# Kernel tuning notes

Hardware: AMD Instinct MI355X
Metric: run time of the kernel (lower is better)

## Reference

```python
import jax, jax.numpy as jnp
import numpy as np

NUM_QUBITS = 6
DIM = 2 ** NUM_QUBITS  # 64


def _u_gate(theta, phi, lam):
    # qiskit U(theta, phi, lam)
    c = jnp.cos(theta / 2).astype(jnp.complex64)
    s = jnp.sin(theta / 2).astype(jnp.complex64)
    ephi = jnp.exp(1j * phi.astype(jnp.complex64))
    elam = jnp.exp(1j * lam.astype(jnp.complex64))
    return jnp.stack([
        jnp.stack([c, -elam * s]),
        jnp.stack([ephi * s, ephi * elam * c]),
    ])


def _p_gate(lam):
    one = jnp.ones((), jnp.complex64)
    return jnp.stack([
        jnp.stack([one, jnp.zeros((), jnp.complex64)]),
        jnp.stack([jnp.zeros((), jnp.complex64), jnp.exp(1j * lam.astype(jnp.complex64))]),
    ])


def _controlled(U):
    # 4x4 matrix in |control, target> basis: block-diag(I2, U)
    return jnp.eye(4, dtype=jnp.complex64).at[2:, 2:].set(U)


_CX = jnp.array([[1, 0, 0, 0], [0, 1, 0, 0], [0, 0, 0, 1], [0, 0, 1, 0]], dtype=jnp.complex64)


def _apply_1q(psi, U, q):
    # psi: (B, 2,2,2,2,2,2); qubit q (qiskit little-endian) -> axis 6-q
    ax = NUM_QUBITS - q
    psi = jnp.moveaxis(psi, ax, -1)
    psi = psi @ U.T
    return jnp.moveaxis(psi, -1, ax)


def _apply_2q(psi, G, qa, qb):
    # G is 4x4 acting on (qa, qb) with index 2*bit(qa)+bit(qb)
    a, b = NUM_QUBITS - qa, NUM_QUBITS - qb
    psi = jnp.moveaxis(psi, (a, b), (-2, -1))
    shp = psi.shape
    psi = (psi.reshape(shp[:-2] + (4,)) @ G.T).reshape(shp)
    return jnp.moveaxis(psi, (-2, -1), (a, b))


def _circuit(features, params):
    # amplitude encoding (qc.initialize with L2 normalization; |0> fallback for zero vec)
    norm = jnp.linalg.norm(features, axis=1, keepdims=True)
    safe = jnp.where(jnp.isclose(norm, 0.0), 1.0, norm)
    e0 = jnp.zeros((1, DIM), features.dtype).at[0, 0].set(1.0)
    psi = jnp.where(jnp.isclose(norm, 0.0), e0, features / safe)
    psi = psi.astype(jnp.complex64).reshape((-1,) + (2,) * NUM_QUBITS)

    def U3(i):
        return _u_gate(params[i], params[i + 1], params[i + 2])

    # layer 1: U on all qubits (params 0..17)
    for q in range(NUM_QUBITS):
        psi = _apply_1q(psi, U3(3 * q), q)
    # cx(2,1); p(18,1); cx(4,3); p(19,3)
    psi = _apply_2q(psi, _CX, 2, 1)
    psi = _apply_1q(psi, _p_gate(params[18]), 1)
    psi = _apply_2q(psi, _CX, 4, 3)
    psi = _apply_1q(psi, _p_gate(params[19]), 3)
    # layer 2: U on [0,1,3,5] (params 20..31)
    idx = 20
    for q in [0, 1, 3, 5]:
        psi = _apply_1q(psi, U3(idx), q)
        idx += 3
    # controlled-U(32..34) ctrl 0 -> tgt 1; controlled-U(35..37) ctrl 3 -> tgt 5
    psi = _apply_2q(psi, _controlled(U3(32)), 0, 1)
    psi = _apply_2q(psi, _controlled(U3(35)), 3, 5)
    # cx(3,1); p(38,1)
    psi = _apply_2q(psi, _CX, 3, 1)
    psi = _apply_1q(psi, _p_gate(params[38]), 1)
    # final: U on [0,1] (39..44); CU(45..47) ctrl 0 -> tgt 1; U on [0,1] (48..53)
    psi = _apply_1q(psi, U3(39), 0)
    psi = _apply_1q(psi, U3(42), 1)
    psi = _apply_2q(psi, _controlled(U3(45)), 0, 1)
    psi = _apply_1q(psi, U3(48), 0)
    psi = _apply_1q(psi, U3(51), 1)

    # observable kron(diag(1,-1), I_32): +1 for index < 32, -1 otherwise (Z on qubit 5)
    probs = jnp.abs(psi.reshape(-1, DIM)) ** 2
    sign = jnp.where(jnp.arange(DIM) < DIM // 2, 1.0, -1.0).astype(jnp.float32)
    return (probs @ sign).astype(jnp.float32)


def setup_inputs() -> dict:
    key = jax.random.key(0)
    kf, kp = jax.random.split(key)
    features = jax.random.normal(kf, (262144, 64), dtype=jnp.float32)
    params = jax.random.uniform(kp, (54,), dtype=jnp.float32) * (0.1 * np.pi)
    return {"features": features, "params": params}


def reference(features, params):
    return _circuit(features, params)
```

## Files before the change

kernel.cpp:

```cpp
#include <hip/hip_runtime.h>

using f32x4  = __attribute__((ext_vector_type(4))) float;
using bf16x8 = __attribute__((ext_vector_type(8))) short;

__device__ inline unsigned short f2bf(float x) {
  unsigned u = __builtin_bit_cast(unsigned, x);
  return (unsigned short)((u + 0x7FFFu + ((u >> 16) & 1u)) >> 16);
}
__device__ inline float2 cmul(float2 a, float2 b) {
  return make_float2(a.x * b.x - a.y * b.y, a.x * b.y + a.y * b.x);
}
__device__ inline float2 cadd(float2 a, float2 b) { return make_float2(a.x + b.x, a.y + b.y); }

__device__ inline void gate1q(float2* psi, int t, int sub, int q,
                              float2 u00, float2 u01, float2 u10, float2 u11) {
  const int bit = 1 << q, mask = bit - 1;
#pragma unroll
  for (int pp = 0; pp < 8; ++pp) {
    int p  = sub * 8 + pp;
    int i0 = ((p & ~mask) << 1) | (p & mask);
    int i1 = i0 | bit;
    float2 a0 = psi[i0 * 64 + t], a1 = psi[i1 * 64 + t];
    psi[i0 * 64 + t] = cadd(cmul(u00, a0), cmul(u01, a1));
    psi[i1 * 64 + t] = cadd(cmul(u10, a0), cmul(u11, a1));
  }
}

__device__ inline void gatec(float2* psi, int t, int sub, int c, int g,
                             float2 v00, float2 v01, float2 v10, float2 v11) {
  const int cb = 1 << c, gb = 1 << g;
  const int lo = (c < g ? c : g), hi = (c < g ? g : c);
  const int mlo = (1 << lo) - 1, mhi = (1 << hi) - 1;
#pragma unroll
  for (int pp = 0; pp < 4; ++pp) {
    int p = sub * 4 + pp;
    int y = ((p & ~mlo) << 1) | (p & mlo);
    y     = ((y & ~mhi) << 1) | (y & mhi);
    int i0 = y | cb;
    int i1 = i0 | gb;
    float2 a0 = psi[i0 * 64 + t], a1 = psi[i1 * 64 + t];
    psi[i0 * 64 + t] = cadd(cmul(v00, a0), cmul(v01, a1));
    psi[i1 * 64 + t] = cadd(cmul(v10, a0), cmul(v11, a1));
  }
}

#define MFMA(A, B, C) __builtin_amdgcn_mfma_f32_16x16x32_bf16(A, B, C, 0, 0, 0)

__global__ __launch_bounds__(256, 3) void qfused(const float* __restrict__ F,
                                                 const float* __restrict__ Pp,
                                                 float* __restrict__ out) {
  __shared__ float2 psi[64 * 64];
  __shared__ __attribute__((aligned(16))) unsigned short Plds[128 * 64];
  __shared__ float tS[54], tC[54], tSh[54], tCh[54];
  __shared__ float sA00;

  const int tid = threadIdx.x;
  const int t = tid & 63, sub = tid >> 6;

  if (tid < 54) {
    float p = Pp[tid];
    tS[tid]  = __sinf(p);
    tC[tid]  = __cosf(p);
    tSh[tid] = __sinf(0.5f * p);
    tCh[tid] = __cosf(0.5f * p);
  }
  for (int idx = tid; idx < 4096; idx += 256)
    psi[idx] = make_float2(((idx >> 6) == (idx & 63)) ? 1.f : 0.f, 0.f);
  __syncthreads();

  float2 u00, u01, u10, u11;
  const float2 Z = make_float2(0.f, 0.f), ONE = make_float2(1.f, 0.f);
  auto U3L = [&](int i) {
    float ch = tCh[i], sh = tSh[i];
    float cp = tC[i + 1], sp = tS[i + 1];
    float cl = tC[i + 2], sl = tS[i + 2];
    u00 = make_float2(ch, 0.f);
    u01 = make_float2(-cl * sh, -sl * sh);
    u10 = make_float2(cp * sh, sp * sh);
    u11 = make_float2((cp * cl - sp * sl) * ch, (cp * sl + sp * cl) * ch);
  };
  auto PH = [&](int i) { return make_float2(tC[i], tS[i]); };

#pragma unroll
  for (int q = 0; q < 6; ++q) {
    U3L(3 * q); gate1q(psi, t, sub, q, u00, u01, u10, u11); __syncthreads();
  }
  gatec(psi, t, sub, 2, 1, Z, ONE, ONE, Z); __syncthreads();
  gate1q(psi, t, sub, 1, ONE, Z, Z, PH(18)); __syncthreads();
  gatec(psi, t, sub, 4, 3, Z, ONE, ONE, Z); __syncthreads();
  gate1q(psi, t, sub, 3, ONE, Z, Z, PH(19)); __syncthreads();
  const int qs[4] = {0, 1, 3, 5};
#pragma unroll
  for (int ii = 0; ii < 4; ++ii) {
    U3L(20 + 3 * ii); gate1q(psi, t, sub, qs[ii], u00, u01, u10, u11); __syncthreads();
  }
  U3L(32); gatec(psi, t, sub, 0, 1, u00, u01, u10, u11); __syncthreads();
  U3L(35); gatec(psi, t, sub, 3, 5, u00, u01, u10, u11); __syncthreads();
  gatec(psi, t, sub, 3, 1, Z, ONE, ONE, Z); __syncthreads();
  gate1q(psi, t, sub, 1, ONE, Z, Z, PH(38)); __syncthreads();
  U3L(39); gate1q(psi, t, sub, 0, u00, u01, u10, u11); __syncthreads();
  U3L(42); gate1q(psi, t, sub, 1, u00, u01, u10, u11); __syncthreads();
  U3L(45); gatec(psi, t, sub, 0, 1, u00, u01, u10, u11); __syncthreads();
  U3L(48); gate1q(psi, t, sub, 0, u00, u01, u10, u11); __syncthreads();
  U3L(51); gate1q(psi, t, sub, 1, u00, u01, u10, u11); __syncthreads();

  if (tid < 64) {
    float2 v = psi[tid * 64];
    float term = (v.x * v.x + v.y * v.y) * (tid < 32 ? 1.f : -1.f);
#pragma unroll
    for (int m = 1; m < 64; m <<= 1) term += __shfl_xor(term, m, 64);
    if (tid == 0) sA00 = term;
  }
  for (int idx = tid; idx < 8192; idx += 256) {
    int r = idx >> 6, j = idx & 63;
    int i = (r < 32) ? r : (r < 96) ? (r - 32) : (r - 64);
    bool im = (r >= 32 && r < 64) || (r >= 96);
    float2 v = psi[i * 64 + j];
    Plds[idx] = f2bf(im ? v.y : v.x);
  }
  __syncthreads();

  const int lane = tid & 63, wid = sub;
  const int g = lane >> 4, c0 = lane & 15;
  const unsigned short* pb = Plds + c0 * 64 + g * 8;
  bf16x8 Bf[8][2];
#pragma unroll
  for (int mt = 0; mt < 8; ++mt) {
    Bf[mt][0] = *(const bf16x8*)(pb + mt * 1024);
    Bf[mt][1] = *(const bf16x8*)(pb + mt * 1024 + 32);
  }
  const float A00 = sA00;

  const int gid   = (int)blockIdx.x * 4 + wid;
  const int start = gid * 5 + (gid < 1024 ? gid : 1024);
  const int count = 5 + (gid < 1024 ? 1 : 0);
  const float* fp = F + (size_t)start * 1024 + (size_t)c0 * 64 + g * 8;

#define LOADT(i, V0, V1, V2, V3) { const float* q_ = fp + (size_t)(i) * 1024; \
    V0 = *(const float4*)(q_); V1 = *(const float4*)(q_ + 4); \
    V2 = *(const float4*)(q_ + 32); V3 = *(const float4*)(q_ + 36); }

#define PROCESS(i, V0, V1, V2, V3) { \
    bf16x8 a0, a1; \
    a0[0] = f2bf(V0.x); a0[1] = f2bf(V0.y); a0[2] = f2bf(V0.z); a0[3] = f2bf(V0.w); \
    a0[4] = f2bf(V1.x); a0[5] = f2bf(V1.y); a0[6] = f2bf(V1.z); a0[7] = f2bf(V1.w); \
    a1[0] = f2bf(V2.x); a1[1] = f2bf(V2.y); a1[2] = f2bf(V2.z); a1[3] = f2bf(V2.w); \
    a1[4] = f2bf(V3.x); a1[5] = f2bf(V3.y); a1[6] = f2bf(V3.z); a1[7] = f2bf(V3.w); \
    f32x4 acc[8]; \
    _Pragma("unroll") \
    for (int mt = 0; mt < 8; ++mt) { \
      acc[mt] = (f32x4){0.f, 0.f, 0.f, 0.f}; \
      acc[mt] = MFMA(Bf[mt][0], a0, acc[mt]); \
      acc[mt] = MFMA(Bf[mt][1], a1, acc[mt]); \
    } \
    float sp_ = 0.f, sm_ = 0.f; \
    _Pragma("unroll") \
    for (int mt = 0; mt < 4; ++mt) { \
      _Pragma("unroll") \
      for (int r = 0; r < 4; ++r) { \
        sp_ = fmaf(acc[mt][r], acc[mt][r], sp_); \
        sm_ = fmaf(acc[mt + 4][r], acc[mt + 4][r], sm_); \
      } \
    } \
    sp_ += __shfl_xor(sp_, 16, 64); sm_ += __shfl_xor(sm_, 16, 64); \
    sp_ += __shfl_xor(sp_, 32, 64); sm_ += __shfl_xor(sm_, 32, 64); \
    if (lane < 16) { \
      float den = sp_ + sm_; \
      out[(size_t)(start + (i)) * 16 + c0] = (den < 1e-30f) ? A00 : (sp_ - sm_) / den; \
    } }

  float4 x0, x1, x2, x3, y0, y1, y2, y3;
  LOADT(0, x0, x1, x2, x3);
#pragma unroll
  for (int i = 0; i < 6; i += 2) {
    if (i >= count) break;
    const bool has2 = (i + 1 < count);
    if (has2) LOADT(i + 1, y0, y1, y2, y3);
    PROCESS(i, x0, x1, x2, x3);
    if (i + 2 < count) LOADT(i + 2, x0, x1, x2, x3);
    if (has2) PROCESS(i + 1, y0, y1, y2, y3);
  }
#undef LOADT
#undef PROCESS
}

extern "C" void kernel_launch(void* const* d_in, const int* in_sizes, int n_in,
                              void* d_out, int out_size, void* d_ws, size_t ws_size,
                              hipStream_t stream) {
  const float* F = (const float*)d_in[0];
  const float* P = (const float*)d_in[1];
  float* out = (float*)d_out;
  qfused<<<768, 256, 0, stream>>>(F, P, out);
}
```

Baseline: 114.3 us.

## Split circuit simulation into single-block kernel and fuse gates into 4x4 unitaries

Before this change, every one of the 768 blocks simulated the full 64x64 circuit unitary. Now one block does it once and writes the bf16 matrix and A00 to global memory, and a second kernel does the MFMA expectation pass. The first layer of 1-qubit gates becomes a closed-form Kronecker product, and neighbouring gate groups are merged into combined 4x4 two-qubit gates, which cuts the number of barriers and LDS passes. The cost is a second kernel launch and a serial single-block step before the main kernel, which now reads the matrix from global memory.

Result: no change. 112.9 us (-1.2%).

```diff
diff --git a/kernel.cpp b/kernel.cpp
--- a/kernel.cpp
+++ b/kernel.cpp
@@ -2,134 +2,177 @@
 
 using f32x4  = __attribute__((ext_vector_type(4))) float;
 using bf16x8 = __attribute__((ext_vector_type(8))) short;
+
+__device__ __attribute__((aligned(16))) unsigned short g_P[128 * 64];
+__device__ float g_A00;
 
 __device__ inline unsigned short f2bf(float x) {
   unsigned u = __builtin_bit_cast(unsigned, x);
   return (unsigned short)((u + 0x7FFFu + ((u >> 16) & 1u)) >> 16);
 }
-__device__ inline float2 cmul(float2 a, float2 b) {
-  return make_float2(a.x * b.x - a.y * b.y, a.x * b.y + a.y * b.x);
-}
-__device__ inline float2 cadd(float2 a, float2 b) { return make_float2(a.x + b.x, a.y + b.y); }
-
-__device__ inline void gate1q(float2* psi, int t, int sub, int q,
-                              float2 u00, float2 u01, float2 u10, float2 u11) {
-  const int bit = 1 << q, mask = bit - 1;
-#pragma unroll
-  for (int pp = 0; pp < 8; ++pp) {
-    int p  = sub * 8 + pp;
-    int i0 = ((p & ~mask) << 1) | (p & mask);
-    int i1 = i0 | bit;
-    float2 a0 = psi[i0 * 64 + t], a1 = psi[i1 * 64 + t];
-    psi[i0 * 64 + t] = cadd(cmul(u00, a0), cmul(u01, a1));
-    psi[i1 * 64 + t] = cadd(cmul(u10, a0), cmul(u11, a1));
-  }
-}
-
-__device__ inline void gatec(float2* psi, int t, int sub, int c, int g,
-                             float2 v00, float2 v01, float2 v10, float2 v11) {
-  const int cb = 1 << c, gb = 1 << g;
-  const int lo = (c < g ? c : g), hi = (c < g ? g : c);
+__device__ inline float2 cmul(float2 x, float2 y) {
+  return make_float2(x.x * y.x - x.y * y.y, x.x * y.y + x.y * y.x);
+}
+__device__ inline float2 cfma(float2 x, float2 y, float2 a) {
+  return make_float2(fmaf(x.x, y.x, fmaf(-x.y, y.y, a.x)),
+                     fmaf(x.x, y.y, fmaf(x.y, y.x, a.y)));
+}
+
+struct u2 { float2 a, b, c, d; };
+struct c4 { float2 m[4][4]; };
+
+__device__ inline u2 mk3(const float* tS, const float* tC,
+                         const float* tSh, const float* tCh, int i) {
+  float ch = tCh[i], sh = tSh[i];
+  float cp = tC[i + 1], sp = tS[i + 1];
+  float cl = tC[i + 2], sl = tS[i + 2];
+  u2 r;
+  r.a = make_float2(ch, 0.f);
+  r.b = make_float2(-cl * sh, -sl * sh);
+  r.c = make_float2(cp * sh, sp * sh);
+  r.d = make_float2((cp * cl - sp * sl) * ch, (cp * sl + sp * cl) * ch);
+  return r;
+}
+__device__ inline c4 kron2(const u2& A, const u2& B) {
+  c4 r;
+  r.m[0][0]=cmul(A.a,B.a); r.m[0][1]=cmul(A.a,B.b); r.m[0][2]=cmul(A.b,B.a); r.m[0][3]=cmul(A.b,B.b);
+  r.m[1][0]=cmul(A.a,B.c); r.m[1][1]=cmul(A.a,B.d); r.m[1][2]=cmul(A.b,B.c); r.m[1][3]=cmul(A.b,B.d);
+  r.m[2][0]=cmul(A.c,B.a); r.m[2][1]=cmul(A.c,B.b); r.m[2][2]=cmul(A.d,B.a); r.m[2][3]=cmul(A.d,B.b);
+  r.m[3][0]=cmul(A.c,B.c); r.m[3][1]=cmul(A.c,B.d); r.m[3][2]=cmul(A.d,B.c); r.m[3][3]=cmul(A.d,B.d);
+  return r;
+}
+__device__ inline c4 mul4(const c4& X, const c4& Y) {
+  c4 r;
+#pragma unroll
+  for (int i = 0; i < 4; ++i)
+#pragma unroll
+    for (int j = 0; j < 4; ++j) {
+      float2 s = make_float2(0.f, 0.f);
+#pragma unroll
+      for (int k = 0; k < 4; ++k) s = cfma(X.m[i][k], Y.m[k][j], s);
+      r.m[i][j] = s;
+    }
+  return r;
+}
+__device__ inline c4 cu4(const u2& U) {
+  c4 r;
+#pragma unroll
+  for (int i = 0; i < 4; ++i)
+#pragma unroll
+    for (int j = 0; j < 4; ++j) r.m[i][j] = make_float2(0.f, 0.f);
+  r.m[0][0] = r.m[1][1] = make_float2(1.f, 0.f);
+  r.m[2][2] = U.a; r.m[2][3] = U.b; r.m[3][2] = U.c; r.m[3][3] = U.d;
+  return r;
+}
+__device__ inline c4 gcxp(float2 e) {
+  c4 r;
+#pragma unroll
+  for (int i = 0; i < 4; ++i)
+#pragma unroll
+    for (int j = 0; j < 4; ++j) r.m[i][j] = make_float2(0.f, 0.f);
+  r.m[0][0] = make_float2(1.f, 0.f); r.m[1][1] = e;
+  r.m[2][3] = make_float2(1.f, 0.f); r.m[3][2] = e;
+  return r;
+}
+
+__device__ inline void g2q(float2* psi, int t, int sub, int qa, int qb, const c4& G) {
+  const int lo = qa < qb ? qa : qb, hi = qa < qb ? qb : qa;
   const int mlo = (1 << lo) - 1, mhi = (1 << hi) - 1;
+  const int dA = (1 << qa) * 64, dB = (1 << qb) * 64;
 #pragma unroll
   for (int pp = 0; pp < 4; ++pp) {
     int p = sub * 4 + pp;
     int y = ((p & ~mlo) << 1) | (p & mlo);
     y     = ((y & ~mhi) << 1) | (y & mhi);
-    int i0 = y | cb;
-    int i1 = i0 | gb;
-    float2 a0 = psi[i0 * 64 + t], a1 = psi[i1 * 64 + t];
-    psi[i0 * 64 + t] = cadd(cmul(v00, a0), cmul(v01, a1));
-    psi[i1 * 64 + t] = cadd(cmul(v10, a0), cmul(v11, a1));
-  }
-}
-
-#define MFMA(A, B, C) __builtin_amdgcn_mfma_f32_16x16x32_bf16(A, B, C, 0, 0, 0)
-
-__global__ __launch_bounds__(256, 3) void qfused(const float* __restrict__ F,
-                                                 const float* __restrict__ Pp,
-                                                 float* __restrict__ out) {
+    int ad = y * 64 + t;
+    float2 a0 = psi[ad], a1 = psi[ad + dB], a2 = psi[ad + dA], a3 = psi[ad + dA + dB];
+    float2 o0 = cfma(G.m[0][3], a3, cfma(G.m[0][2], a2, cfma(G.m[0][1], a1, cmul(G.m[0][0], a0))));
+    float2 o1 = cfma(G.m[1][3], a3, cfma(G.m[1][2], a2, cfma(G.m[1][1], a1, cmul(G.m[1][0], a0))));
+    float2 o2 = cfma(G.m[2][3], a3, cfma(G.m[2][2], a2, cfma(G.m[2][1], a1, cmul(G.m[2][0], a0))));
+    float2 o3 = cfma(G.m[3][3], a3, cfma(G.m[3][2], a2, cfma(G.m[3][1], a1, cmul(G.m[3][0], a0))));
+    psi[ad] = o0; psi[ad + dB] = o1; psi[ad + dA] = o2; psi[ad + dA + dB] = o3;
+  }
+}
+__device__ inline float2 pick(const u2& U, int bi, int bt) {
+  return bi ? (bt ? U.d : U.c) : (bt ? U.b : U.a);
+}
+
+__global__ __launch_bounds__(256) void sim_kernel(const float* __restrict__ Pp) {
   __shared__ float2 psi[64 * 64];
-  __shared__ __attribute__((aligned(16))) unsigned short Plds[128 * 64];
   __shared__ float tS[54], tC[54], tSh[54], tCh[54];
-  __shared__ float sA00;
-
-  const int tid = threadIdx.x;
-  const int t = tid & 63, sub = tid >> 6;
-
+  const int tid = threadIdx.x, t = tid & 63, sub = tid >> 6;
   if (tid < 54) {
     float p = Pp[tid];
-    tS[tid]  = __sinf(p);
-    tC[tid]  = __cosf(p);
-    tSh[tid] = __sinf(0.5f * p);
-    tCh[tid] = __cosf(0.5f * p);
-  }
-  for (int idx = tid; idx < 4096; idx += 256)
-    psi[idx] = make_float2(((idx >> 6) == (idx & 63)) ? 1.f : 0.f, 0.f);
+    tS[tid] = __sinf(p);  tC[tid] = __cosf(p);
+    tSh[tid] = __sinf(0.5f * p); tCh[tid] = __cosf(0.5f * p);
+  }
   __syncthreads();
 
-  float2 u00, u01, u10, u11;
-  const float2 Z = make_float2(0.f, 0.f), ONE = make_float2(1.f, 0.f);
-  auto U3L = [&](int i) {
-    float ch = tCh[i], sh = tSh[i];
-    float cp = tC[i + 1], sp = tS[i + 1];
-    float cl = tC[i + 2], sl = tS[i + 2];
-    u00 = make_float2(ch, 0.f);
-    u01 = make_float2(-cl * sh, -sl * sh);
-    u10 = make_float2(cp * sh, sp * sh);
-    u11 = make_float2((cp * cl - sp * sl) * ch, (cp * sl + sp * cl) * ch);
-  };
-  auto PH = [&](int i) { return make_float2(tC[i], tS[i]); };
-
-#pragma unroll
-  for (int q = 0; q < 6; ++q) {
-    U3L(3 * q); gate1q(psi, t, sub, q, u00, u01, u10, u11); __syncthreads();
-  }
-  gatec(psi, t, sub, 2, 1, Z, ONE, ONE, Z); __syncthreads();
-  gate1q(psi, t, sub, 1, ONE, Z, Z, PH(18)); __syncthreads();
-  gatec(psi, t, sub, 4, 3, Z, ONE, ONE, Z); __syncthreads();
-  gate1q(psi, t, sub, 3, ONE, Z, Z, PH(19)); __syncthreads();
-  const int qs[4] = {0, 1, 3, 5};
-#pragma unroll
-  for (int ii = 0; ii < 4; ++ii) {
-    U3L(20 + 3 * ii); gate1q(psi, t, sub, qs[ii], u00, u01, u10, u11); __syncthreads();
-  }
-  U3L(32); gatec(psi, t, sub, 0, 1, u00, u01, u10, u11); __syncthreads();
-  U3L(35); gatec(psi, t, sub, 3, 5, u00, u01, u10, u11); __syncthreads();
-  gatec(psi, t, sub, 3, 1, Z, ONE, ONE, Z); __syncthreads();
-  gate1q(psi, t, sub, 1, ONE, Z, Z, PH(38)); __syncthreads();
-  U3L(39); gate1q(psi, t, sub, 0, u00, u01, u10, u11); __syncthreads();
-  U3L(42); gate1q(psi, t, sub, 1, u00, u01, u10, u11); __syncthreads();
-  U3L(45); gatec(psi, t, sub, 0, 1, u00, u01, u10, u11); __syncthreads();
-  U3L(48); gate1q(psi, t, sub, 0, u00, u01, u10, u11); __syncthreads();
-  U3L(51); gate1q(psi, t, sub, 1, u00, u01, u10, u11); __syncthreads();
+  {
+    u2 L0 = mk3(tS, tC, tSh, tCh, 0),  L1 = mk3(tS, tC, tSh, tCh, 3);
+    u2 L2 = mk3(tS, tC, tSh, tCh, 6),  L3 = mk3(tS, tC, tSh, tCh, 9);
+    u2 L4 = mk3(tS, tC, tSh, tCh, 12), L5 = mk3(tS, tC, tSh, tCh, 15);
+#pragma unroll
+    for (int e = 0; e < 16; ++e) {
+      int idx = tid + 256 * e;
+      int i = idx >> 6, tt = idx & 63;
+      float2 f = pick(L0, i & 1, tt & 1);
+      f = cmul(f, pick(L1, (i >> 1) & 1, (tt >> 1) & 1));
+      f = cmul(f, pick(L2, (i >> 2) & 1, (tt >> 2) & 1));
+      f = cmul(f, pick(L3, (i >> 3) & 1, (tt >> 3) & 1));
+      f = cmul(f, pick(L4, (i >> 4) & 1, (tt >> 4) & 1));
+      f = cmul(f, pick(L5, (i >> 5) & 1, (tt >> 5) & 1));
+      psi[idx] = f;
+    }
+  }
+  __syncthreads();
+  auto E = [&](int i) { return make_float2(tC[i], tS[i]); };
+  { c4 G = gcxp(E(18)); g2q(psi, t, sub, 2, 1, G); } __syncthreads();
+  { c4 G = gcxp(E(19)); g2q(psi, t, sub, 4, 3, G); } __syncthreads();
+  { c4 G = mul4(cu4(mk3(tS, tC, tSh, tCh, 32)),
+                kron2(mk3(tS, tC, tSh, tCh, 20), mk3(tS, tC, tSh, tCh, 23)));
+    g2q(psi, t, sub, 0, 1, G); } __syncthreads();
+  { c4 G = mul4(cu4(mk3(tS, tC, tSh, tCh, 35)),
+                kron2(mk3(tS, tC, tSh, tCh, 26), mk3(tS, tC, tSh, tCh, 29)));
+    g2q(psi, t, sub, 3, 5, G); } __syncthreads();
+  { c4 G = gcxp(E(38)); g2q(psi, t, sub, 3, 1, G); } __syncthreads();
+  { c4 G = mul4(kron2(mk3(tS, tC, tSh, tCh, 48), mk3(tS, tC, tSh, tCh, 51)),
+                mul4(cu4(mk3(tS, tC, tSh, tCh, 45)),
+                     kron2(mk3(tS, tC, tSh, tCh, 39), mk3(tS, tC, tSh, tCh, 42))));
+    g2q(psi, t, sub, 0, 1, G); } __syncthreads();
 
   if (tid < 64) {
     float2 v = psi[tid * 64];
     float term = (v.x * v.x + v.y * v.y) * (tid < 32 ? 1.f : -1.f);
 #pragma unroll
     for (int m = 1; m < 64; m <<= 1) term += __shfl_xor(term, m, 64);
-    if (tid == 0) sA00 = term;
+    if (tid == 0) g_A00 = term;
   }
   for (int idx = tid; idx < 8192; idx += 256) {
     int r = idx >> 6, j = idx & 63;
     int i = (r < 32) ? r : (r < 96) ? (r - 32) : (r - 64);
     bool im = (r >= 32 && r < 64) || (r >= 96);
     float2 v = psi[i * 64 + j];
-    Plds[idx] = f2bf(im ? v.y : v.x);
-  }
-  __syncthreads();
-
-  const int lane = tid & 63, wid = sub;
+    g_P[idx] = f2bf(im ? v.y : v.x);
+  }
+}
+
+#define MFMA(A, B, C) __builtin_amdgcn_mfma_f32_16x16x32_bf16(A, B, C, 0, 0, 0)
+
+__global__ __launch_bounds__(256, 3) void qexp(const float* __restrict__ F,
+                                               float* __restrict__ out) {
+  const int tid = threadIdx.x;
+  const int lane = tid & 63, wid = tid >> 6;
   const int g = lane >> 4, c0 = lane & 15;
-  const unsigned short* pb = Plds + c0 * 64 + g * 8;
+
+  const unsigned short* pb = g_P + c0 * 64 + g * 8;
   bf16x8 Bf[8][2];
 #pragma unroll
   for (int mt = 0; mt < 8; ++mt) {
     Bf[mt][0] = *(const bf16x8*)(pb + mt * 1024);
     Bf[mt][1] = *(const bf16x8*)(pb + mt * 1024 + 32);
   }
-  const float A00 = sA00;
+  const float A00 = g_A00;
 
   const int gid   = (int)blockIdx.x * 4 + wid;
   const int start = gid * 5 + (gid < 1024 ? gid : 1024);
@@ -190,5 +233,6 @@
   const float* F = (const float*)d_in[0];
   const float* P = (const float*)d_in[1];
   float* out = (float*)d_out;
-  qfused<<<768, 256, 0, stream>>>(F, P, out);
-}
+  sim_kernel<<<1, 256, 0, stream>>>(P);
+  qexp<<<768, 256, 0, stream>>>(F, out);
+}
```
